# Optimization experiments

Measured on AMD Instinct MI355X. Metric: run time of the kernel, lower is better.

The kernel has to match this reference:

```python
import jax, jax.numpy as jnp
import numpy as np

B, L, D = 32768, 256, 16  # batch, chain length, bond dim; physical dim d=2


def setup_inputs() -> dict:
    key = jax.random.key(0)
    k_phi, k_first, k_mid, k_last = jax.random.split(key, 4)
    scale = 1.0 / np.sqrt(2.0 * D)  # variance-preserving chain
    phi_batch = jax.random.normal(k_phi, (B, L, 2), dtype=jnp.float32)
    core_first = jax.random.normal(k_first, (2, D), dtype=jnp.float32) * scale
    cores_mid = jax.random.normal(k_mid, (L - 2, D, 2, D), dtype=jnp.float32) * scale
    core_last = jax.random.normal(k_last, (D, 2), dtype=jnp.float32) * scale
    out_bias = jnp.zeros((), dtype=jnp.float32)
    return {
        "phi_batch": phi_batch,
        "core_first": core_first,
        "cores_mid": cores_mid,
        "core_last": core_last,
        "out_bias": out_bias,
    }


def reference(phi_batch, core_first, cores_mid, core_last, out_bias):
    # MPS / tensor-train contraction, batched over samples.
    # Each sample contracts feature vectors phi[i] (len-2) into the physical
    # index of core i, then chains the resulting D x D matrices via a
    # left-to-right bond-space matvec (what cotengra would find per-sample).
    # v0: [B, D] = phi[:,0] contracted with first core [2, D]
    v0 = jnp.einsum("bp,pd->bd", phi_batch[:, 0], core_first)

    # middle features, scan-major layout: [L-2, B, 2]
    phis_mid = jnp.swapaxes(phi_batch[:, 1:-1], 0, 1)

    def step(v, xs):
        phi_t, core = xs  # phi_t: [B, 2], core: [D, 2, D]
        # contract bond then physical index; never materialize [B, D, D]
        u = jnp.einsum("bq,qpr->bpr", v, core)   # [B, 2, D]
        v_new = jnp.einsum("bp,bpr->br", phi_t, u)  # [B, D]
        return v_new, None

    v, _ = jax.lax.scan(step, v0, (phis_mid, cores_mid))

    # close the chain with last core [D, 2] and last feature [B, 2]
    out = jnp.einsum("bq,qp,bp->b", v, core_last, phi_batch[:, -1])
    return out + out_bias
```

## Files before the change

kernel.cpp:

```cpp
#include <hip/hip_runtime.h>
#include <stdint.h>


typedef short  bf16x8 __attribute__((ext_vector_type(8)));
typedef float  f32x4  __attribute__((ext_vector_type(4)));
typedef int    i32x4  __attribute__((ext_vector_type(4)));
typedef unsigned int u32;

#define NPF 64
#define NPB 63
#define BWD_OFF (NPF*4*64)
#define NCHUNK 32

#define PACK_HI(hi, lo) ((int)__builtin_amdgcn_perm((u32)(hi), (u32)(lo), 0x07060302u))

__device__ __forceinline__ u32 rne_bump(u32 u){ return u + 0x7FFFu + ((u >> 16) & 1u); }

__device__ __forceinline__ void async16(const void* g, void* l){
  __builtin_amdgcn_global_load_lds(
    (const __attribute__((address_space(1))) u32*)(uintptr_t)g,
    (__attribute__((address_space(3))) u32*)(uintptr_t)l, 16, 0, 0);
}

__global__ void build_pair_frags(const float* __restrict__ cm, i32x4* __restrict__ ws)
{
  __shared__ float Ca[512], Cb[512];
  const int bid = blockIdx.x;
  const bool fwd = bid < NPF;
  const int j  = fwd ? bid : bid - NPF;
  const int ta = fwd ? 2*j     : 252 - 2*j;
  const int tb = fwd ? 2*j + 1 : 253 - 2*j;
  {
    const float* A = cm + ta*512;
    const float* B = cm + tb*512;
    for (int i = threadIdx.x; i < 512; i += 256){ Ca[i] = A[i]; Cb[i] = B[i]; }
  }
  __syncthreads();
  const int f    = threadIdx.x >> 6;
  const int lane = threadIdx.x & 63;
  const int m    = lane & 15;
  const int g    = lane >> 4;
  const int p    = f >> 1, q = f & 1;
  u32 hi[4], lo[4];
  #pragma unroll
  for (int x = 0; x < 4; ++x){
    const int cq = 4*g + x;
    float acc = 0.f;
    #pragma unroll
    for (int r = 0; r < 16; ++r){
      const float a = fwd ? Ca[cq*32 + p*16 + r] : Ca[m*32 + p*16 + r];
      const float b = fwd ? Cb[r*32 + q*16 + m]  : Cb[r*32 + q*16 + cq];
      acc = fmaf(a, b, acc);
    }
    const u32 u  = __float_as_uint(acc);
    const u32 aa = rne_bump(u);
    const float hf = __uint_as_float(aa & 0xFFFF0000u);
    const u32 bb = rne_bump(__float_as_uint(acc - hf));
    hi[x] = aa >> 16; lo[x] = bb >> 16;
  }
  i32x4 w;
  w[0] = (int)(hi[0] | (hi[1] << 16));
  w[1] = (int)(hi[2] | (hi[3] << 16));
  w[2] = (int)(lo[0] | (lo[1] << 16));
  w[3] = (int)(lo[2] | (lo[3] << 16));
  ws[(fwd ? 0 : BWD_OFF) + (j*4 + f)*64 + lane] = w;
}

__global__ __launch_bounds__(256, 4) void mps_chain(
  const float* __restrict__ phi,
  const float* __restrict__ core_first,
  const float* __restrict__ core_last,
  const float* __restrict__ bias,
  const i32x4* __restrict__ ws,
  float* __restrict__ out)
{
  const int lane = threadIdx.x & 63;
  const int wv   = threadIdx.x >> 6;
  const int b0   = blockIdx.x * 32;
  const int n    = lane & 15;
  const int g    = lane >> 4;
  const int half = wv & 1;
  const int s_in = half*16 + n;
  const bool isFwd = (wv < 2);
  const int dirIdx = isFwd ? 0 : 1;

  __shared__ i32x4 frag[2][2][2][4][64];
  __shared__ float phL[2][2][2][4][16][4];

  const float* phiRow = phi + (size_t)(b0 + s_in) * 512;

  const float* phiDma = phi + (size_t)(b0 + 16*half + (lane & 15)) * 512
                            + (lane >> 4) * 4;
  const i32x4* wsD = isFwd ? ws : (ws + BWD_OFF);

  auto issue_dma = [&](int cn, int buf){
    int pr = 2*cn + half;
    if (!isFwd && pr > NPB-1) pr = NPB-1;
    const i32x4* base = wsD + pr*4*64 + lane;
    #pragma unroll
    for (int f = 0; f < 4; ++f)
      async16(base + f*64, &frag[dirIdx][buf][half][f][0]);
    const int W = isFwd ? 4*cn : (248 - 4*cn);
    async16(phiDma + 2*W, &phL[dirIdx][buf][half][0][0][0]);
  };

  float v[4];
  i32x4 bfr;

  auto make_bfrag = [&](){
    const u32 u0 = __float_as_uint(v[0]), u1 = __float_as_uint(v[1]);
    const u32 u2 = __float_as_uint(v[2]), u3 = __float_as_uint(v[3]);
    const float l0 = v[0] - __uint_as_float(u0 & 0xFFFF0000u);
    const float l1 = v[1] - __uint_as_float(u1 & 0xFFFF0000u);
    const float l2 = v[2] - __uint_as_float(u2 & 0xFFFF0000u);
    const float l3 = v[3] - __uint_as_float(u3 & 0xFFFF0000u);
    bfr[0] = PACK_HI(u1, u0);
    bfr[1] = PACK_HI(u3, u2);
    bfr[2] = PACK_HI(__float_as_uint(l1), __float_as_uint(l0));
    bfr[3] = PACK_HI(__float_as_uint(l3), __float_as_uint(l2));
  };

  auto pair_step = [&](const i32x4& G0, const i32x4& G1, const i32x4& G2,
                       const i32x4& G3, float2 cA, float2 cB){
    const float c00 = cA.x*cB.x, c01 = cA.x*cB.y;
    const float c10 = cA.y*cB.x, c11 = cA.y*cB.y;
    i32x4 sw; sw[0]=bfr[2]; sw[1]=bfr[3]; sw[2]=bfr[0]; sw[3]=bfr[1];
    const bf16x8 bh = __builtin_bit_cast(bf16x8, bfr);
    const bf16x8 bs = __builtin_bit_cast(bf16x8, sw);
    const f32x4 z = {0.f,0.f,0.f,0.f};
    f32x4 a00 = __builtin_amdgcn_mfma_f32_16x16x32_bf16(__builtin_bit_cast(bf16x8,G0), bh, z, 0,0,0);
    a00 = __builtin_amdgcn_mfma_f32_16x16x32_bf16(__builtin_bit_cast(bf16x8,G0), bs, a00, 0,0,0);
    f32x4 a01 = __builtin_amdgcn_mfma_f32_16x16x32_bf16(__builtin_bit_cast(bf16x8,G1), bh, z, 0,0,0);
    a01 = __builtin_amdgcn_mfma_f32_16x16x32_bf16(__builtin_bit_cast(bf16x8,G1), bs, a01, 0,0,0);
    f32x4 a10 = __builtin_amdgcn_mfma_f32_16x16x32_bf16(__builtin_bit_cast(bf16x8,G2), bh, z, 0,0,0);
    a10 = __builtin_amdgcn_mfma_f32_16x16x32_bf16(__builtin_bit_cast(bf16x8,G2), bs, a10, 0,0,0);
    f32x4 a11 = __builtin_amdgcn_mfma_f32_16x16x32_bf16(__builtin_bit_cast(bf16x8,G3), bh, z, 0,0,0);
    a11 = __builtin_amdgcn_mfma_f32_16x16x32_bf16(__builtin_bit_cast(bf16x8,G3), bs, a11, 0,0,0);
    #pragma unroll
    for (int i2 = 0; i2 < 4; ++i2)
      v[i2] = c00*a00[i2] + c01*a01[i2] + c10*a10[i2] + c11*a11[i2];
    make_bfrag();
  };

  if (isFwd){
    const float2 ph0 = *(const float2*)phiRow;
    #pragma unroll
    for (int reg = 0; reg < 4; ++reg){
      const int r = g*4 + reg;
      v[reg] = ph0.x * core_first[r] + ph0.y * core_first[16 + r];
    }
  } else {
    const float2 phL2 = *(const float2*)(phiRow + 510);
    #pragma unroll
    for (int reg = 0; reg < 4; ++reg){
      const int r = g*4 + reg;
      v[reg] = phL2.x * core_last[2*r] + phL2.y * core_last[2*r + 1];
    }
  }
  make_bfrag();

  issue_dma(0, 0);
  __syncthreads();

  #pragma unroll 1
  for (int c = 0; c < NCHUNK; ++c){
    const int buf = c & 1;
    if (c + 1 < NCHUNK) issue_dma(c + 1, buf ^ 1);

    const float* pb = &phL[dirIdx][buf][half][0][n][0];
    const float2 xA0 = *(const float2*)(pb + (isFwd ?   2 : 130));
    const float2 xB0 = *(const float2*)(pb + (isFwd ?  64 : 192));
    const float2 xA1 = *(const float2*)(pb + 66);
    const float2 xB1 = *(const float2*)(pb + 128);

    {
      const i32x4 G0 = frag[dirIdx][buf][0][0][lane];
      const i32x4 G1 = frag[dirIdx][buf][0][1][lane];
      const i32x4 G2 = frag[dirIdx][buf][0][2][lane];
      const i32x4 G3 = frag[dirIdx][buf][0][3][lane];
      pair_step(G0, G1, G2, G3, xA0, xB0);
    }
    if (isFwd || (2*c + 1) < NPB){
      const i32x4 G0 = frag[dirIdx][buf][1][0][lane];
      const i32x4 G1 = frag[dirIdx][buf][1][1][lane];
      const i32x4 G2 = frag[dirIdx][buf][1][2][lane];
      const i32x4 G3 = frag[dirIdx][buf][1][3][lane];
      pair_step(G0, G1, G2, G3, xA1, xB1);
    }
    __syncthreads();
  }

  float* red = (float*)&frag[0][0][0][0][0];
  *(float4*)&red[(dirIdx*32 + s_in)*20 + 4*g] =
      make_float4(v[0], v[1], v[2], v[3]);
  __syncthreads();
  if (threadIdx.x < 32){
    const int s = threadIdx.x;
    float acc = bias[0];
    #pragma unroll
    for (int qq = 0; qq < 16; ++qq)
      acc += red[s*20 + qq] * red[(32 + s)*20 + qq];
    out[b0 + s] = acc;
  }
}

extern "C" void kernel_launch(void* const* d_in, const int* in_sizes, int n_in,
                              void* d_out, int out_size, void* d_ws, size_t ws_size,
                              hipStream_t stream)
{
  const float* phi  = (const float*)d_in[0];
  const float* cf   = (const float*)d_in[1];
  const float* cm   = (const float*)d_in[2];
  const float* cl   = (const float*)d_in[3];
  const float* bias = (const float*)d_in[4];
  i32x4* ws = (i32x4*)d_ws;

  build_pair_frags<<<NPF + NPB, 256, 0, stream>>>(cm, ws);
  mps_chain<<<1024, 256, 0, stream>>>(phi, cf, cl, bias, ws, (float*)d_out);
}
```

Before: 138.7 us.

## Deepen async prefetch with a four-slot fragment ring and per-pair barriers

Replaces the double-buffered per-chunk DMA with a four-slot ring of pair fragments, and a separate double buffer for phi. Each half-block now loads half of every pair's fragments, and a fragment is issued three pair-steps ahead. Explicit vmcnt waits plus raw s_barrier calls guard each pair-step, in place of one __syncthreads per chunk. MFMA sequences are wrapped in s_setprio to favour matrix issue. The aim is to hide global-to-LDS latency across the serial chain, at the cost of twice as many barriers and fragile hand-counted vmcnt bookkeeping.

```diff
diff --git a/kernel.cpp b/kernel.cpp
--- a/kernel.cpp
+++ b/kernel.cpp
@@ -84,7 +84,7 @@
   const bool isFwd = (wv < 2);
   const int dirIdx = isFwd ? 0 : 1;
 
-  __shared__ i32x4 frag[2][2][2][4][64];
+  __shared__ i32x4 frag[2][4][4][64];
   __shared__ float phL[2][2][2][4][16][4];
 
   const float* phiRow = phi + (size_t)(b0 + s_in) * 512;
@@ -92,16 +92,19 @@
   const float* phiDma = phi + (size_t)(b0 + 16*half + (lane & 15)) * 512
                             + (lane >> 4) * 4;
   const i32x4* wsD = isFwd ? ws : (ws + BWD_OFF);
-
-  auto issue_dma = [&](int cn, int buf){
-    int pr = 2*cn + half;
-    if (!isFwd && pr > NPB-1) pr = NPB-1;
-    const i32x4* base = wsD + pr*4*64 + lane;
-    #pragma unroll
-    for (int f = 0; f < 4; ++f)
-      async16(base + f*64, &frag[dirIdx][buf][half][f][0]);
+  const int maxPr  = isFwd ? NPF - 1 : NPB - 1;
+  const i32x4* wsLane = wsD + (2*half)*64 + lane;
+
+  auto FRAG = [&](int j){
+    const int pr = j > maxPr ? maxPr : j;
+    const i32x4* s = wsLane + pr*256;
+    i32x4* d = &frag[dirIdx][j & 3][2*half][0];
+    async16(s,      d);
+    async16(s + 64, d + 64);
+  };
+  auto PHI = [&](int cn){
     const int W = isFwd ? 4*cn : (248 - 4*cn);
-    async16(phiDma + 2*W, &phL[dirIdx][buf][half][0][0][0]);
+    async16(phiDma + 2*W, &phL[dirIdx][cn & 1][half][0][0][0]);
   };
 
   float v[4];
@@ -120,14 +123,18 @@
     bfr[3] = PACK_HI(__float_as_uint(l3), __float_as_uint(l2));
   };
 
-  auto pair_step = [&](const i32x4& G0, const i32x4& G1, const i32x4& G2,
-                       const i32x4& G3, float2 cA, float2 cB){
+  auto pair_step = [&](const i32x4* Gb, float2 cA, float2 cB){
+    const i32x4 G0 = Gb[0];
+    const i32x4 G1 = Gb[64];
+    const i32x4 G2 = Gb[128];
+    const i32x4 G3 = Gb[192];
     const float c00 = cA.x*cB.x, c01 = cA.x*cB.y;
     const float c10 = cA.y*cB.x, c11 = cA.y*cB.y;
     i32x4 sw; sw[0]=bfr[2]; sw[1]=bfr[3]; sw[2]=bfr[0]; sw[3]=bfr[1];
     const bf16x8 bh = __builtin_bit_cast(bf16x8, bfr);
     const bf16x8 bs = __builtin_bit_cast(bf16x8, sw);
     const f32x4 z = {0.f,0.f,0.f,0.f};
+    __builtin_amdgcn_s_setprio(1);
     f32x4 a00 = __builtin_amdgcn_mfma_f32_16x16x32_bf16(__builtin_bit_cast(bf16x8,G0), bh, z, 0,0,0);
     a00 = __builtin_amdgcn_mfma_f32_16x16x32_bf16(__builtin_bit_cast(bf16x8,G0), bs, a00, 0,0,0);
     f32x4 a01 = __builtin_amdgcn_mfma_f32_16x16x32_bf16(__builtin_bit_cast(bf16x8,G1), bh, z, 0,0,0);
@@ -136,6 +143,7 @@
     a10 = __builtin_amdgcn_mfma_f32_16x16x32_bf16(__builtin_bit_cast(bf16x8,G2), bs, a10, 0,0,0);
     f32x4 a11 = __builtin_amdgcn_mfma_f32_16x16x32_bf16(__builtin_bit_cast(bf16x8,G3), bh, z, 0,0,0);
     a11 = __builtin_amdgcn_mfma_f32_16x16x32_bf16(__builtin_bit_cast(bf16x8,G3), bs, a11, 0,0,0);
+    __builtin_amdgcn_s_setprio(0);
     #pragma unroll
     for (int i2 = 0; i2 < 4; ++i2)
       v[i2] = c00*a00[i2] + c01*a01[i2] + c10*a10[i2] + c11*a11[i2];
@@ -159,38 +167,43 @@
   }
   make_bfrag();
 
-  issue_dma(0, 0);
-  __syncthreads();
+  PHI(0); FRAG(0); FRAG(1); PHI(1); FRAG(2);
+  __builtin_amdgcn_sched_barrier(0);
 
   #pragma unroll 1
   for (int c = 0; c < NCHUNK; ++c){
-    const int buf = c & 1;
-    if (c + 1 < NCHUNK) issue_dma(c + 1, buf ^ 1);
-
-    const float* pb = &phL[dirIdx][buf][half][0][n][0];
+    const int bufp = c & 1;
+
+    asm volatile("s_waitcnt vmcnt(5)" ::: "memory");
+    __builtin_amdgcn_sched_barrier(0);
+    __builtin_amdgcn_s_barrier();
+    __builtin_amdgcn_sched_barrier(0);
+
+    const float* pb = &phL[dirIdx][bufp][half][0][n][0];
     const float2 xA0 = *(const float2*)(pb + (isFwd ?   2 : 130));
     const float2 xB0 = *(const float2*)(pb + (isFwd ?  64 : 192));
     const float2 xA1 = *(const float2*)(pb + 66);
     const float2 xB1 = *(const float2*)(pb + 128);
 
-    {
-      const i32x4 G0 = frag[dirIdx][buf][0][0][lane];
-      const i32x4 G1 = frag[dirIdx][buf][0][1][lane];
-      const i32x4 G2 = frag[dirIdx][buf][0][2][lane];
-      const i32x4 G3 = frag[dirIdx][buf][0][3][lane];
-      pair_step(G0, G1, G2, G3, xA0, xB0);
-    }
-    if (isFwd || (2*c + 1) < NPB){
-      const i32x4 G0 = frag[dirIdx][buf][1][0][lane];
-      const i32x4 G1 = frag[dirIdx][buf][1][1][lane];
-      const i32x4 G2 = frag[dirIdx][buf][1][2][lane];
-      const i32x4 G3 = frag[dirIdx][buf][1][3][lane];
-      pair_step(G0, G1, G2, G3, xA1, xB1);
-    }
-    __syncthreads();
-  }
-
-  float* red = (float*)&frag[0][0][0][0][0];
+    pair_step(&frag[dirIdx][(2*c) & 3][0][lane], xA0, xB0);
+    FRAG(2*c + 3);
+    __builtin_amdgcn_sched_barrier(0);
+
+    asm volatile("s_waitcnt vmcnt(5)" ::: "memory");
+    __builtin_amdgcn_sched_barrier(0);
+    __builtin_amdgcn_s_barrier();
+    __builtin_amdgcn_sched_barrier(0);
+
+    if (isFwd || (2*c + 1) < NPB)
+      pair_step(&frag[dirIdx][(2*c + 1) & 3][0][lane], xA1, xB1);
+    PHI(c + 2);
+    FRAG(2*c + 4);
+    __builtin_amdgcn_sched_barrier(0);
+  }
+
+  __syncthreads();
+
+  float* red = (float*)&frag[0][0][0][0];
   *(float4*)&red[(dirIdx*32 + s_in)*20 + 4*g] =
       make_float4(v[0], v[1], v[2], v[3]);
   __syncthreads();
```

Measured after the change: 137.6 us. About the same (-0.8%).

## Replace LDS async staging with register prefetch and bpermute phi shuffles

Applied to the files above, without the earlier changes.

Drops the global_load_lds double-buffered staging of core fragments and phi values, along with the per-chunk __syncthreads. Each wave now loads its pair fragments straight into registers one pair ahead, and prefetches a phi vector that lanes exchange with ds_bpermute. It also raises wave priority around the MFMA sequence. This removes block-wide barriers and LDS round trips from the serial chain, at the cost of more VGPRs and global-load latency exposed on each step.

```diff
diff --git a/kernel.cpp b/kernel.cpp
--- a/kernel.cpp
+++ b/kernel.cpp
@@ -10,17 +10,10 @@
 #define NPF 64
 #define NPB 63
 #define BWD_OFF (NPF*4*64)
-#define NCHUNK 32
 
 #define PACK_HI(hi, lo) ((int)__builtin_amdgcn_perm((u32)(hi), (u32)(lo), 0x07060302u))
 
 __device__ __forceinline__ u32 rne_bump(u32 u){ return u + 0x7FFFu + ((u >> 16) & 1u); }
-
-__device__ __forceinline__ void async16(const void* g, void* l){
-  __builtin_amdgcn_global_load_lds(
-    (const __attribute__((address_space(1))) u32*)(uintptr_t)g,
-    (__attribute__((address_space(3))) u32*)(uintptr_t)l, 16, 0, 0);
-}
 
 __global__ void build_pair_frags(const float* __restrict__ cm, i32x4* __restrict__ ws)
 {
@@ -84,25 +77,23 @@
   const bool isFwd = (wv < 2);
   const int dirIdx = isFwd ? 0 : 1;
 
-  __shared__ i32x4 frag[2][2][2][4][64];
-  __shared__ float phL[2][2][2][4][16][4];
+  __shared__ float red[64*20];
 
   const float* phiRow = phi + (size_t)(b0 + s_in) * 512;
 
-  const float* phiDma = phi + (size_t)(b0 + 16*half + (lane & 15)) * 512
+  const float* phiSrc = phi + (size_t)(b0 + 16*half + (lane & 15)) * 512
                             + (lane >> 4) * 4;
-  const i32x4* wsD = isFwd ? ws : (ws + BWD_OFF);
-
-  auto issue_dma = [&](int cn, int buf){
-    int pr = 2*cn + half;
-    if (!isFwd && pr > NPB-1) pr = NPB-1;
-    const i32x4* base = wsD + pr*4*64 + lane;
-    #pragma unroll
-    for (int f = 0; f < 4; ++f)
-      async16(base + f*64, &frag[dirIdx][buf][half][f][0]);
-    const int W = isFwd ? 4*cn : (248 - 4*cn);
-    async16(phiDma + 2*W, &phL[dirIdx][buf][half][0][0][0]);
-  };
+
+  const i32x4* wsD    = isFwd ? ws : (ws + BWD_OFF);
+  const int    maxPr  = isFwd ? NPF - 1 : NPB - 1;
+  const i32x4* wsLane = wsD + lane;
+
+  const int qtF  = isFwd ? 0 : 1;
+  const int aQ   = ((lane & 15) + 16*qtF) << 2;
+  const int adrA0 = isFwd ? aQ       : aQ + 64;
+  const int adrB0 = isFwd ? aQ + 64  : aQ + 128;
+  const int adrA1 = isFwd ? aQ + 64  : aQ;
+  const int adrB1 = isFwd ? aQ + 128 : aQ + 64;
 
   float v[4];
   i32x4 bfr;
@@ -128,6 +119,7 @@
     const bf16x8 bh = __builtin_bit_cast(bf16x8, bfr);
     const bf16x8 bs = __builtin_bit_cast(bf16x8, sw);
     const f32x4 z = {0.f,0.f,0.f,0.f};
+    __builtin_amdgcn_s_setprio(1);
     f32x4 a00 = __builtin_amdgcn_mfma_f32_16x16x32_bf16(__builtin_bit_cast(bf16x8,G0), bh, z, 0,0,0);
     a00 = __builtin_amdgcn_mfma_f32_16x16x32_bf16(__builtin_bit_cast(bf16x8,G0), bs, a00, 0,0,0);
     f32x4 a01 = __builtin_amdgcn_mfma_f32_16x16x32_bf16(__builtin_bit_cast(bf16x8,G1), bh, z, 0,0,0);
@@ -136,6 +128,7 @@
     a10 = __builtin_amdgcn_mfma_f32_16x16x32_bf16(__builtin_bit_cast(bf16x8,G2), bs, a10, 0,0,0);
     f32x4 a11 = __builtin_amdgcn_mfma_f32_16x16x32_bf16(__builtin_bit_cast(bf16x8,G3), bh, z, 0,0,0);
     a11 = __builtin_amdgcn_mfma_f32_16x16x32_bf16(__builtin_bit_cast(bf16x8,G3), bs, a11, 0,0,0);
+    __builtin_amdgcn_s_setprio(0);
     #pragma unroll
     for (int i2 = 0; i2 < 4; ++i2)
       v[i2] = c00*a00[i2] + c01*a01[i2] + c10*a10[i2] + c11*a11[i2];
@@ -159,38 +152,53 @@
   }
   make_bfrag();
 
-  issue_dma(0, 0);
-  __syncthreads();
+  i32x4 A0, A1, A2, A3;
+  i32x4 B0, B1, B2, B3;
+  f32x4 phiC, phiN;
+
+  {
+    const i32x4* s = wsLane;
+    A0 = s[0]; A1 = s[64]; A2 = s[128]; A3 = s[192];
+  }
+  {
+    const i32x4* s = wsLane + 256;
+    B0 = s[0]; B1 = s[64]; B2 = s[128]; B3 = s[192];
+  }
+  phiC = *(const f32x4*)(phiSrc + (isFwd ? 0 : 496));
+  phiN = *(const f32x4*)(phiSrc + (isFwd ? 8 : 488));
 
   #pragma unroll 1
-  for (int c = 0; c < NCHUNK; ++c){
-    const int buf = c & 1;
-    if (c + 1 < NCHUNK) issue_dma(c + 1, buf ^ 1);
-
-    const float* pb = &phL[dirIdx][buf][half][0][n][0];
-    const float2 xA0 = *(const float2*)(pb + (isFwd ?   2 : 130));
-    const float2 xB0 = *(const float2*)(pb + (isFwd ?  64 : 192));
-    const float2 xA1 = *(const float2*)(pb + 66);
-    const float2 xB1 = *(const float2*)(pb + 128);
-
+  for (int c = 0; c < 32; ++c){
+    auto S = [&](int e, int adr)->float {
+      return __int_as_float(__builtin_amdgcn_ds_bpermute(adr, __float_as_int(phiC[e])));
+    };
+    const float2 xA0 = make_float2(S(2, adrA0), S(3, adrA0));
+    const float2 xB0 = make_float2(S(0, adrB0), S(1, adrB0));
+    const float2 xA1 = make_float2(S(2, adrA1), S(3, adrA1));
+    const float2 xB1 = make_float2(S(0, adrB1), S(1, adrB1));
+
+    pair_step(A0, A1, A2, A3, xA0, xB0);
     {
-      const i32x4 G0 = frag[dirIdx][buf][0][0][lane];
-      const i32x4 G1 = frag[dirIdx][buf][0][1][lane];
-      const i32x4 G2 = frag[dirIdx][buf][0][2][lane];
-      const i32x4 G3 = frag[dirIdx][buf][0][3][lane];
-      pair_step(G0, G1, G2, G3, xA0, xB0);
-    }
-    if (isFwd || (2*c + 1) < NPB){
-      const i32x4 G0 = frag[dirIdx][buf][1][0][lane];
-      const i32x4 G1 = frag[dirIdx][buf][1][1][lane];
-      const i32x4 G2 = frag[dirIdx][buf][1][2][lane];
-      const i32x4 G3 = frag[dirIdx][buf][1][3][lane];
-      pair_step(G0, G1, G2, G3, xA1, xB1);
-    }
-    __syncthreads();
-  }
-
-  float* red = (float*)&frag[0][0][0][0][0];
+      const int j = 2*c + 2;
+      const i32x4* s = wsLane + (j > maxPr ? maxPr : j) * 256;
+      A0 = s[0]; A1 = s[64]; A2 = s[128]; A3 = s[192];
+    }
+
+    if (isFwd || (2*c + 1) < NPB)
+      pair_step(B0, B1, B2, B3, xA1, xB1);
+    {
+      const int j = 2*c + 3;
+      const i32x4* s = wsLane + (j > maxPr ? maxPr : j) * 256;
+      B0 = s[0]; B1 = s[64]; B2 = s[128]; B3 = s[192];
+    }
+
+    phiC = phiN;
+    {
+      const int cc = (c + 2 > 31) ? 31 : (c + 2);
+      phiN = *(const f32x4*)(phiSrc + (isFwd ? 8*cc : 496 - 8*cc));
+    }
+  }
+
   *(float4*)&red[(dirIdx*32 + s_in)*20 + 4*g] =
       make_float4(v[0], v[1], v[2], v[3]);
   __syncthreads();
```

New measurement: 148.4 us. 1.07x slower.
